# Optimization experiments

Measured on AMD Instinct MI355X. Metric: run time of the kernel, lower is better.

The kernel has to match this reference:

```python
import jax, jax.numpy as jnp
import numpy as np

B = 32768
F = 256
H = 8


def setup_inputs() -> dict:
    key = jax.random.key(0)
    ks = jax.random.split(key, 6)
    input_tensor = jax.random.normal(ks[0], (B, F), dtype=jnp.float32)
    # Per-feature MLP params: Dense(1->8), Dense(8->8), Dense(8->1, no bias)
    W1 = jax.random.normal(ks[1], (F, H), dtype=jnp.float32) * 0.5   # [F, 8] (input dim 1 folded)
    b1 = jax.random.normal(ks[2], (F, H), dtype=jnp.float32) * 0.1
    W2 = jax.random.normal(ks[3], (F, H, H), dtype=jnp.float32) * (1.0 / np.sqrt(H))
    b2 = jax.random.normal(ks[4], (F, H), dtype=jnp.float32) * 0.1
    W3 = jax.random.normal(ks[5], (F, H), dtype=jnp.float32) * (1.0 / np.sqrt(H))  # [F, 8] (output dim 1 folded)
    return {"input_tensor": input_tensor, "W1": W1, "b1": b1, "W2": W2, "b2": b2, "W3": W3}


def reference(input_tensor, W1, b1, W2, b2, W3):
    # Batched over features instead of a Python loop over F tiny MLPs.
    # h1: [B, F, H] = relu(x * W1 + b1), scalar input per feature
    h1 = jax.nn.relu(input_tensor[:, :, None] * W1[None, :, :] + b1[None, :, :])
    # h2: [B, F, H]
    h2 = jax.nn.relu(jnp.einsum('bfh,fhk->bfk', h1, W2) + b2[None, :, :])
    # per-feature scalar contribution w: [B, F]
    w = jnp.einsum('bfh,fh->bf', h2, W3)
    output = jnp.sum(w, axis=1, keepdims=True)  # [B, 1]
    return (output, w)
```

## Files before the change

### kernel.cpp

```cpp
#include <hip/hip_runtime.h>

#define NB 32768
#define NF 256
#define NH 8
#define RPB 32


typedef float f4 __attribute__((ext_vector_type(4)));
typedef __attribute__((address_space(1))) const unsigned int gu32;
typedef __attribute__((address_space(3))) unsigned int lu32;

__global__ __launch_bounds__(256, 3) void NAM_49314814493074_kernel(
    const float* __restrict__ input,
    const float* __restrict__ W1,
    const float* __restrict__ b1,
    const float* __restrict__ W2,
    const float* __restrict__ b2,
    const float* __restrict__ W3,
    float* __restrict__ out_sum,
    float* __restrict__ out_w)
{
    __shared__ float xs[RPB][NF];

    const int f    = threadIdx.x;
    const int wave = f >> 6;
    const int lane = f & 63;
    const int row0 = blockIdx.x * RPB;

    {
        const float* g = input + (size_t)row0 * NF + wave * 64 + lane;
        float* l = &xs[0][wave * 64];
        #pragma unroll
        for (int r = 0; r < RPB; ++r) {
            __builtin_amdgcn_global_load_lds((gu32*)(g + (size_t)r * NF),
                                             (lu32*)(l + r * NF), 4, 0, 0);
        }
    }

    f4 w1a, w1b, b1a, b1b, b2a, b2b, w3a, w3b, w2v[16];
    {
        const f4* pW1 = reinterpret_cast<const f4*>(W1 + (size_t)f * NH);
        const f4* pB1 = reinterpret_cast<const f4*>(b1 + (size_t)f * NH);
        const f4* pB2 = reinterpret_cast<const f4*>(b2 + (size_t)f * NH);
        const f4* pW3 = reinterpret_cast<const f4*>(W3 + (size_t)f * NH);
        const f4* pW2 = reinterpret_cast<const f4*>(W2 + (size_t)f * NH * NH);
        w1a = pW1[0]; w1b = pW1[1];
        b1a = pB1[0]; b1b = pB1[1];
        b2a = pB2[0]; b2b = pB2[1];
        w3a = pW3[0]; w3b = pW3[1];
        #pragma unroll
        for (int i = 0; i < 16; ++i) w2v[i] = pW2[i];
    }
    asm volatile("" : "+v"(w1a), "+v"(w1b), "+v"(b1a), "+v"(b1b),
                      "+v"(b2a), "+v"(b2b), "+v"(w3a), "+v"(w3b));
    asm volatile("" : "+v"(w2v[0]), "+v"(w2v[1]), "+v"(w2v[2]), "+v"(w2v[3]),
                      "+v"(w2v[4]), "+v"(w2v[5]), "+v"(w2v[6]), "+v"(w2v[7]),
                      "+v"(w2v[8]), "+v"(w2v[9]), "+v"(w2v[10]), "+v"(w2v[11]),
                      "+v"(w2v[12]), "+v"(w2v[13]), "+v"(w2v[14]), "+v"(w2v[15]));

    __syncthreads();

    #pragma unroll
    for (int r = 0; r < RPB; ++r) {
        const float x = xs[r][f];

        float h1[NH];
        #pragma unroll
        for (int h = 0; h < NH; ++h)
            h1[h] = fmaxf(fmaf(x, (h < 4 ? w1a[h] : w1b[h - 4]),
                                  (h < 4 ? b1a[h] : b1b[h - 4])), 0.0f);

        float acc[NH];
        #pragma unroll
        for (int k = 0; k < NH; ++k)
            acc[k] = fmaf(h1[0], w2v[(k >> 2)][k & 3],
                          (k < 4 ? b2a[k] : b2b[k - 4]));
        #pragma unroll
        for (int h = 1; h < NH; ++h) {
            #pragma unroll
            for (int k = 0; k < NH; ++k)
                acc[k] = fmaf(h1[h], w2v[h * 2 + (k >> 2)][k & 3], acc[k]);
        }

        float s = 0.0f;
        #pragma unroll
        for (int k = 0; k < NH; ++k)
            s = fmaf(fmaxf(acc[k], 0.0f), (k < 4 ? w3a[k] : w3b[k - 4]), s);

        xs[r][f] = s;
    }

    __syncthreads();

    #pragma unroll
    for (int rr = 0; rr < RPB / 4; ++rr) {
        const int r = wave * (RPB / 4) + rr;
        const float4 q = reinterpret_cast<const float4*>(&xs[r][0])[lane];
        reinterpret_cast<float4*>(out_w + (size_t)(row0 + r) * NF)[lane] = q;
        float v = q.x + q.y + q.z + q.w;
        #pragma unroll
        for (int off = 32; off > 0; off >>= 1)
            v += __shfl_xor(v, off, 64);
        if (lane == 0)
            out_sum[row0 + r] = v;
    }
}

extern "C" void kernel_launch(void* const* d_in, const int* in_sizes, int n_in,
                              void* d_out, int out_size, void* d_ws, size_t ws_size,
                              hipStream_t stream) {
    const float* input = (const float*)d_in[0];
    const float* W1    = (const float*)d_in[1];
    const float* b1    = (const float*)d_in[2];
    const float* W2    = (const float*)d_in[3];
    const float* b2    = (const float*)d_in[4];
    const float* W3    = (const float*)d_in[5];

    float* out = (float*)d_out;
    float* out_sum = out;
    float* out_w   = out + NB;

    dim3 grid(NB / RPB);
    dim3 block(NF);
    NAM_49314814493074_kernel<<<grid, block, 0, stream>>>(
        input, W1, b1, W2, b2, W3, out_sum, out_w);
}
```

Measured before the change: 109.7 us.

## Split features across blocks, register-tile rows, and reduce sums with atomics

The kernel now gives each block 64 features by 64 rows, with 4 waves each covering 16 rows. Each thread processes its rows in tiles of 4 and reloads the weights from cache on every tile instead of pinning all of them in registers. The LDS staging and the coalesced float4 write-back are dropped in favour of direct strided per-thread loads and stores, and the row sums use a wave reduction plus atomicAdd after a memset. The aim is lower register pressure and higher occupancy, at the cost of atomics, an extra memset launch, and repeated weight loads.

Result: slower. 116.1 us (+5.8%).

```diff
diff --git a/kernel.cpp b/kernel.cpp
--- a/kernel.cpp
+++ b/kernel.cpp
@@ -3,14 +3,17 @@
 #define NB 32768
 #define NF 256
 #define NH 8
-#define RPB 32
+#define FPB 64
+#define RPB 64
+#define NRG 4
+#define RPG (RPB / NRG)
+#define RT 4
+#define NT (RPG / RT)
 
 
 typedef float f4 __attribute__((ext_vector_type(4)));
-typedef __attribute__((address_space(1))) const unsigned int gu32;
-typedef __attribute__((address_space(3))) unsigned int lu32;
 
-__global__ __launch_bounds__(256, 3) void NAM_49314814493074_kernel(
+__global__ __launch_bounds__(256, 4) void NAM_49314814493074_kernel(
     const float* __restrict__ input,
     const float* __restrict__ W1,
     const float* __restrict__ b1,
@@ -20,89 +23,84 @@
     float* __restrict__ out_sum,
     float* __restrict__ out_w)
 {
-    __shared__ float xs[RPB][NF];
+    const int t    = threadIdx.x;
+    const int lane = t & 63;
+    const int rg   = t >> 6;
+    const int fb   = blockIdx.x & 3;
+    const int rb   = blockIdx.x >> 2;
+    const int f    = fb * FPB + lane;
+    const int row0 = rb * RPB + rg * RPG;
 
-    const int f    = threadIdx.x;
-    const int wave = f >> 6;
-    const int lane = f & 63;
-    const int row0 = blockIdx.x * RPB;
+    const float* xin  = input + (size_t)row0 * NF + f;
+    float*       wout = out_w + (size_t)row0 * NF + f;
 
-    {
-        const float* g = input + (size_t)row0 * NF + wave * 64 + lane;
-        float* l = &xs[0][wave * 64];
+    const f4* pW1 = reinterpret_cast<const f4*>(W1 + (size_t)f * NH);
+    const f4* pB1 = reinterpret_cast<const f4*>(b1 + (size_t)f * NH);
+    const f4* pB2 = reinterpret_cast<const f4*>(b2 + (size_t)f * NH);
+    const f4* pW3 = reinterpret_cast<const f4*>(W3 + (size_t)f * NH);
+    const f4* pW2 = reinterpret_cast<const f4*>(W2 + (size_t)f * NH * NH);
+
+    #pragma unroll 1
+    for (int tile = 0; tile < NT; ++tile) {
+        const int rbase = tile * RT;
+
+        float xv[RT];
         #pragma unroll
-        for (int r = 0; r < RPB; ++r) {
-            __builtin_amdgcn_global_load_lds((gu32*)(g + (size_t)r * NF),
-                                             (lu32*)(l + r * NF), 4, 0, 0);
+        for (int r = 0; r < RT; ++r)
+            xv[r] = xin[(size_t)(rbase + r) * NF];
+
+        f4 w1a = pW1[0], w1b = pW1[1];
+        f4 b1a = pB1[0], b1b = pB1[1];
+
+        float acc[RT][NH];
+
+        {
+            f4 wa = pW2[0], wb = pW2[1];
+            #pragma unroll
+            for (int r = 0; r < RT; ++r) {
+                const float h1 = fmaxf(fmaf(xv[r], w1a[0], b1a[0]), 0.0f);
+                #pragma unroll
+                for (int k = 0; k < 4; ++k) {
+                    acc[r][k]     = h1 * wa[k];
+                    acc[r][4 + k] = h1 * wb[k];
+                }
+            }
         }
-    }
-
-    f4 w1a, w1b, b1a, b1b, b2a, b2b, w3a, w3b, w2v[16];
-    {
-        const f4* pW1 = reinterpret_cast<const f4*>(W1 + (size_t)f * NH);
-        const f4* pB1 = reinterpret_cast<const f4*>(b1 + (size_t)f * NH);
-        const f4* pB2 = reinterpret_cast<const f4*>(b2 + (size_t)f * NH);
-        const f4* pW3 = reinterpret_cast<const f4*>(W3 + (size_t)f * NH);
-        const f4* pW2 = reinterpret_cast<const f4*>(W2 + (size_t)f * NH * NH);
-        w1a = pW1[0]; w1b = pW1[1];
-        b1a = pB1[0]; b1b = pB1[1];
-        b2a = pB2[0]; b2b = pB2[1];
-        w3a = pW3[0]; w3b = pW3[1];
-        #pragma unroll
-        for (int i = 0; i < 16; ++i) w2v[i] = pW2[i];
-    }
-    asm volatile("" : "+v"(w1a), "+v"(w1b), "+v"(b1a), "+v"(b1b),
-                      "+v"(b2a), "+v"(b2b), "+v"(w3a), "+v"(w3b));
-    asm volatile("" : "+v"(w2v[0]), "+v"(w2v[1]), "+v"(w2v[2]), "+v"(w2v[3]),
-                      "+v"(w2v[4]), "+v"(w2v[5]), "+v"(w2v[6]), "+v"(w2v[7]),
-                      "+v"(w2v[8]), "+v"(w2v[9]), "+v"(w2v[10]), "+v"(w2v[11]),
-                      "+v"(w2v[12]), "+v"(w2v[13]), "+v"(w2v[14]), "+v"(w2v[15]));
-
-    __syncthreads();
-
-    #pragma unroll
-    for (int r = 0; r < RPB; ++r) {
-        const float x = xs[r][f];
-
-        float h1[NH];
-        #pragma unroll
-        for (int h = 0; h < NH; ++h)
-            h1[h] = fmaxf(fmaf(x, (h < 4 ? w1a[h] : w1b[h - 4]),
-                                  (h < 4 ? b1a[h] : b1b[h - 4])), 0.0f);
-
-        float acc[NH];
-        #pragma unroll
-        for (int k = 0; k < NH; ++k)
-            acc[k] = fmaf(h1[0], w2v[(k >> 2)][k & 3],
-                          (k < 4 ? b2a[k] : b2b[k - 4]));
         #pragma unroll
         for (int h = 1; h < NH; ++h) {
+            const f4 wa = pW2[2 * h], wb = pW2[2 * h + 1];
+            const float w1h = (h < 4) ? w1a[h] : w1b[h - 4];
+            const float b1h = (h < 4) ? b1a[h] : b1b[h - 4];
             #pragma unroll
-            for (int k = 0; k < NH; ++k)
-                acc[k] = fmaf(h1[h], w2v[h * 2 + (k >> 2)][k & 3], acc[k]);
+            for (int r = 0; r < RT; ++r) {
+                const float h1 = fmaxf(fmaf(xv[r], w1h, b1h), 0.0f);
+                #pragma unroll
+                for (int k = 0; k < 4; ++k) {
+                    acc[r][k]     = fmaf(h1, wa[k], acc[r][k]);
+                    acc[r][4 + k] = fmaf(h1, wb[k], acc[r][4 + k]);
+                }
+            }
         }
 
-        float s = 0.0f;
+        const f4 b2a = pB2[0], b2b = pB2[1];
+        const f4 w3a = pW3[0], w3b = pW3[1];
         #pragma unroll
-        for (int k = 0; k < NH; ++k)
-            s = fmaf(fmaxf(acc[k], 0.0f), (k < 4 ? w3a[k] : w3b[k - 4]), s);
+        for (int r = 0; r < RT; ++r) {
+            float s = 0.0f;
+            #pragma unroll
+            for (int k = 0; k < 4; ++k) {
+                s = fmaf(fmaxf(acc[r][k]     + b2a[k], 0.0f), w3a[k], s);
+                s = fmaf(fmaxf(acc[r][4 + k] + b2b[k], 0.0f), w3b[k], s);
+            }
+            wout[(size_t)(rbase + r) * NF] = s;
 
-        xs[r][f] = s;
-    }
-
-    __syncthreads();
-
-    #pragma unroll
-    for (int rr = 0; rr < RPB / 4; ++rr) {
-        const int r = wave * (RPB / 4) + rr;
-        const float4 q = reinterpret_cast<const float4*>(&xs[r][0])[lane];
-        reinterpret_cast<float4*>(out_w + (size_t)(row0 + r) * NF)[lane] = q;
-        float v = q.x + q.y + q.z + q.w;
-        #pragma unroll
-        for (int off = 32; off > 0; off >>= 1)
-            v += __shfl_xor(v, off, 64);
-        if (lane == 0)
-            out_sum[row0 + r] = v;
+            float v = s;
+            #pragma unroll
+            for (int off = 32; off > 0; off >>= 1)
+                v += __shfl_xor(v, off, 64);
+            if (lane == 0)
+                atomicAdd(&out_sum[row0 + rbase + r], v);
+        }
     }
 }
 
@@ -120,8 +118,10 @@
     float* out_sum = out;
     float* out_w   = out + NB;
 
-    dim3 grid(NB / RPB);
-    dim3 block(NF);
+    hipMemsetAsync(out_sum, 0, NB * sizeof(float), stream);
+
+    dim3 grid((NF / FPB) * (NB / RPB));
+    dim3 block(256);
     NAM_49314814493074_kernel<<<grid, block, 0, stream>>>(
         input, W1, b1, W2, b2, W3, out_sum, out_w);
 }
```
